# Kernel optimization log

Measured on AMD Instinct MI355X. Metric: run time of the kernel, lower is better.

## Reference

```python
import jax, jax.numpy as jnp
import numpy as np

N_NODES = 50000
N_EDGES = 200000
N_GRAPHS = 256
D_IN = 100
H = 384
STEPS = 4
EPS = 1e-5  # torch BatchNorm1d default eps


def setup_inputs() -> dict:
    key = jax.random.key(0)
    ks = jax.random.split(key, 16)
    def nrm(k, shape, s=0.05):
        return jax.random.normal(k, shape, jnp.float32) * s
    return {
        "x": jax.random.normal(ks[0], (N_NODES, D_IN), jnp.float32),
        "edge_index": jax.random.randint(ks[1], (2, N_EDGES), 0, N_NODES, jnp.int32),
        "batch": jnp.sort(jax.random.randint(ks[2], (N_NODES,), 0, N_GRAPHS, jnp.int32)),
        "w_in": nrm(ks[3], (D_IN, H)), "b_in": jnp.zeros((H,), jnp.float32),
        "bn1_g": jnp.ones((H,), jnp.float32), "bn1_b": jnp.zeros((H,), jnp.float32),
        "ggc_w": nrm(ks[4], (STEPS, H, H)),
        "gru_wih": nrm(ks[5], (3 * H, H)), "gru_whh": nrm(ks[6], (3 * H, H)),
        "gru_bih": jnp.zeros((3 * H,), jnp.float32), "gru_bhh": jnp.zeros((3 * H,), jnp.float32),
        "bn2_g": jnp.ones((H,), jnp.float32), "bn2_b": jnp.zeros((H,), jnp.float32),
        "att_w": nrm(ks[7], (H, 1)), "att_b": jnp.zeros((1,), jnp.float32),
        "fc1_w": nrm(ks[8], (H, H)), "fc1_b": jnp.zeros((H,), jnp.float32),
        "bn3_g": jnp.ones((H,), jnp.float32), "bn3_b": jnp.zeros((H,), jnp.float32),
        "fc2_w": nrm(ks[9], (H, H // 2)), "fc2_b": jnp.zeros((H // 2,), jnp.float32),
        "bn4_g": jnp.ones((H // 2,), jnp.float32), "bn4_b": jnp.zeros((H // 2,), jnp.float32),
        "fc3_w": nrm(ks[10], (H // 2, 2)), "fc3_b": jnp.zeros((2,), jnp.float32),
    }


def _bn(x, g, b):
    # training-mode BatchNorm1d: biased batch stats over dim 0
    m = x.mean(0)
    v = x.var(0)
    return (x - m) * jax.lax.rsqrt(v + EPS) * g + b


def reference(x, edge_index, batch, w_in, b_in, bn1_g, bn1_b, ggc_w,
              gru_wih, gru_whh, gru_bih, gru_bhh, bn2_g, bn2_b,
              att_w, att_b, fc1_w, fc1_b, bn3_g, bn3_b,
              fc2_w, fc2_b, bn4_g, bn4_b, fc3_w, fc3_b):
    h = jax.nn.relu(_bn(x @ w_in + b_in, bn1_g, bn1_b))  # [N, H]
    skip = h
    src, dst = edge_index[0], edge_index[1]
    # GatedGraphConv: per-step linear -> scatter-add over edges -> GRUCell
    for i in range(STEPS):
        m = h @ ggc_w[i]                                   # [N, H]
        agg = jax.ops.segment_sum(m[src], dst, num_segments=N_NODES)
        gi = agg @ gru_wih.T + gru_bih                     # [N, 3H]
        gh = h @ gru_whh.T + gru_bhh
        ir, iz, inn = jnp.split(gi, 3, axis=1)
        hr, hz, hn = jnp.split(gh, 3, axis=1)
        r = jax.nn.sigmoid(ir + hr)
        z = jax.nn.sigmoid(iz + hz)
        n = jnp.tanh(inn + r * hn)
        h = (1.0 - z) * n + z * h
    h = jax.nn.relu(_bn(h, bn2_g, bn2_b) + skip)
    # per-graph attention pooling (segment softmax + weighted segment sum)
    logits = (h @ att_w + att_b)[:, 0]                     # [N]
    seg_max = jax.ops.segment_max(logits, batch, num_segments=N_GRAPHS)
    e = jnp.exp(logits - seg_max[batch])
    denom = jax.ops.segment_sum(e, batch, num_segments=N_GRAPHS)
    w = e / denom[batch]
    pooled = jax.ops.segment_sum(w[:, None] * h, batch, num_segments=N_GRAPHS)  # [G, H]
    y = jax.nn.relu(_bn(pooled @ fc1_w + fc1_b, bn3_g, bn3_b))
    y = jax.nn.relu(_bn(y @ fc2_w + fc2_b, bn4_g, bn4_b))
    return y @ fc3_w + fc3_b                               # [G, 2]
```

## Files before the change

kernel.cpp:

```cpp
#include <hip/hip_runtime.h>
#include <math.h>

#define N_NODESC 50000
#define N_EDGESC 200000
#define N_GRAPHSC 256
#define D_INC 100
#define HD 384
#define STEPSC 4
#define BN_EPS 1e-5f

#define FPSCALE 4194304.0f
#define FPINV   (1.0f / 4194304.0f)

#define STATS_ROWS 512
#define STATS_BLOCKS 98

typedef _Float16 h8v __attribute__((ext_vector_type(8)));
typedef _Float16 h4v __attribute__((ext_vector_type(4)));
typedef float f4v __attribute__((ext_vector_type(4)));

static __device__ __forceinline__ float sigmoidf_(float x) { return 1.0f / (1.0f + expf(-x)); }

static __device__ __forceinline__ f4v mfma3(h8v ah, h8v al, h8v bh, h8v bl, f4v c) {
    c = __builtin_amdgcn_mfma_f32_16x16x32_f16(ah, bh, c, 0, 0, 0);
    c = __builtin_amdgcn_mfma_f32_16x16x32_f16(ah, bl, c, 0, 0, 0);
    c = __builtin_amdgcn_mfma_f32_16x16x32_f16(al, bh, c, 0, 0, 0);
    return c;
}

static __device__ __forceinline__ void gload_lds16(const _Float16* g, _Float16* l) {
    __builtin_amdgcn_global_load_lds(
        (const __attribute__((address_space(1))) unsigned int*)g,
        (__attribute__((address_space(3))) unsigned int*)l, 16, 0, 0);
}

static __device__ __forceinline__ int xcd_swz(int orig, int nwg) {
    const int q = nwg >> 3, r = nwg & 7;
    const int xcd = orig & 7, idx = orig >> 3;
    return (xcd < r ? xcd * (q + 1) : r * (q + 1) + (xcd - r) * q) + idx;
}

__global__ __launch_bounds__(256) void gemm64(const float* __restrict__ A,
                                              const float* __restrict__ B,
                                              const float* __restrict__ bias,
                                              float* __restrict__ C,
                                              int M, int K, int N) {
    __shared__ float As[16][68];
    __shared__ float Bs[16][68];
    const int tid = threadIdx.x;
    const int tx = tid & 15, ty = tid >> 4;
    const int m0 = blockIdx.y << 6, n0 = blockIdx.x << 6;
    const int ar = tid >> 2, ac4 = tid & 3;
    const int br = tid >> 4, bc4 = tid & 15;
    float acc[4][4] = {};
    for (int k0 = 0; k0 < K; k0 += 16) {
        float4 av = make_float4(0.f, 0.f, 0.f, 0.f);
        const int arow = m0 + ar, ak = k0 + (ac4 << 2);
        if (arow < M && ak < K) av = *(const float4*)(A + (size_t)arow * K + ak);
        As[(ac4 << 2) + 0][ar] = av.x;
        As[(ac4 << 2) + 1][ar] = av.y;
        As[(ac4 << 2) + 2][ar] = av.z;
        As[(ac4 << 2) + 3][ar] = av.w;
        float4 bv = make_float4(0.f, 0.f, 0.f, 0.f);
        const int bk = k0 + br;
        if (bk < K) bv = *(const float4*)(B + (size_t)bk * N + n0 + (bc4 << 2));
        *(float4*)&Bs[br][bc4 << 2] = bv;
        __syncthreads();
#pragma unroll
        for (int kk = 0; kk < 16; ++kk) {
            const float4 a = *(const float4*)&As[kk][ty << 2];
            const float4 b = *(const float4*)&Bs[kk][tx << 2];
            const float aarr[4] = {a.x, a.y, a.z, a.w};
            const float barr[4] = {b.x, b.y, b.z, b.w};
#pragma unroll
            for (int i = 0; i < 4; ++i)
#pragma unroll
                for (int j = 0; j < 4; ++j) acc[i][j] = fmaf(aarr[i], barr[j], acc[i][j]);
        }
        __syncthreads();
    }
#pragma unroll
    for (int i = 0; i < 4; ++i) {
        const int row = m0 + (ty << 2) + i;
        if (row >= M) continue;
        const int col0 = n0 + (tx << 2);
        float4 out;
        out.x = acc[i][0]; out.y = acc[i][1]; out.z = acc[i][2]; out.w = acc[i][3];
        if (bias) {
            out.x += bias[col0 + 0]; out.y += bias[col0 + 1];
            out.z += bias[col0 + 2]; out.w += bias[col0 + 3];
        }
        *(float4*)(C + (size_t)row * N + col0) = out;
    }
}


__global__ __launch_bounds__(256) void pack_gru_w(const float* __restrict__ w,
                                                  _Float16* __restrict__ PH,
                                                  _Float16* __restrict__ PL) {
    const int i = blockIdx.x * 256 + threadIdx.x;
    if (i >= 3 * 24 * 12 * 64) return;
    const int l = i & 63;
    const int kc = (i >> 6) % 12;
    const int jt = ((i >> 6) / 12) % 24;
    const int g = (i >> 6) / (12 * 24);
    const int row = g * HD + jt * 16 + (l & 15);
    const int k0 = kc * 32 + ((l >> 4) << 3);
    const float* s = w + (size_t)row * HD + k0;
    h8v hi, lo;
#pragma unroll
    for (int e = 0; e < 8; ++e) {
        const float v = s[e];
        hi[e] = (_Float16)v;
        lo[e] = (_Float16)(v - (float)hi[e]);
    }
    *(h8v*)(PH + (size_t)i * 8) = hi;
    *(h8v*)(PL + (size_t)i * 8) = lo;
}

__global__ __launch_bounds__(256) void pack_ggc_w(const float* __restrict__ w,
                                                  _Float16* __restrict__ PH,
                                                  _Float16* __restrict__ PL) {
    const int i = blockIdx.x * 256 + threadIdx.x;
    if (i >= STEPSC * 24 * 12 * 64) return;
    const int l = i & 63;
    const int kc = (i >> 6) % 12;
    const int jt = ((i >> 6) / 12) % 24;
    const int s = (i >> 6) / (12 * 24);
    const int n = jt * 16 + (l & 15);
    const int k0 = kc * 32 + ((l >> 4) << 3);
    h8v hi, lo;
#pragma unroll
    for (int e = 0; e < 8; ++e) {
        const float v = w[((size_t)s * HD + k0 + e) * HD + n];
        hi[e] = (_Float16)v;
        lo[e] = (_Float16)(v - (float)hi[e]);
    }
    *(h8v*)(PH + (size_t)i * 8) = hi;
    *(h8v*)(PL + (size_t)i * 8) = lo;
}

__global__ void deg_count(const int* __restrict__ dst, int* __restrict__ deg) {
    const int e = blockIdx.x * 256 + threadIdx.x;
    if (e < N_EDGESC) atomicAdd(&deg[dst[e]], 1);
}

__global__ __launch_bounds__(1024) void scan_deg(const int* __restrict__ deg,
                                                 int* __restrict__ offs) {
    __shared__ int sums[1024];
    const int t = threadIdx.x;
    const int CH = (N_NODESC + 1023) / 1024;
    const int base = t * CH;
    int s = 0;
    for (int i = 0; i < CH; ++i) {
        const int idx = base + i;
        if (idx < N_NODESC) s += deg[idx];
    }
    sums[t] = s;
    __syncthreads();
    for (int o = 1; o < 1024; o <<= 1) {
        const int v = (t >= o) ? sums[t - o] : 0;
        __syncthreads();
        sums[t] += v;
        __syncthreads();
    }
    int run = (t > 0) ? sums[t - 1] : 0;
    for (int i = 0; i < CH; ++i) {
        const int idx = base + i;
        if (idx < N_NODESC) {
            offs[idx] = run;
            run += deg[idx];
        }
    }
    if (t == 1023) offs[N_NODESC] = run;
}

__global__ void fill_csr(const int* __restrict__ src, const int* __restrict__ dst,
                         const int* __restrict__ offs, int* __restrict__ cursor,
                         int* __restrict__ esrc) {
    const int e = blockIdx.x * 256 + threadIdx.x;
    if (e >= N_EDGESC) return;
    const int d = dst[e];
    const int pos = atomicAdd(&cursor[d], 1);
    esrc[offs[d] + pos] = src[e];
}

__global__ __launch_bounds__(256) void gather_agg(const float* __restrict__ m,
                                                  const int* __restrict__ offs,
                                                  const int* __restrict__ esrc,
                                                  int* __restrict__ aggi) {
    const int gid = blockIdx.x * 256 + threadIdx.x;
    const int n = gid / 96;
    const int c = gid % 96;
    if (n >= N_NODESC) return;
    const int beg = offs[n], end = offs[n + 1];
    int4 acc = make_int4(0, 0, 0, 0);
    for (int i = beg; i < end; ++i) {
        const int s = esrc[i];
        const float4 v = *(const float4*)(m + (size_t)s * HD + (c << 2));
        acc.x += __float2int_rn(v.x * FPSCALE);
        acc.y += __float2int_rn(v.y * FPSCALE);
        acc.z += __float2int_rn(v.z * FPSCALE);
        acc.w += __float2int_rn(v.w * FPSCALE);
    }
    *(int4*)(aggi + (size_t)n * HD + (c << 2)) = acc;
}

__global__ __launch_bounds__(256) void ggc_lds(const _Float16* __restrict__ hH,
                                               const _Float16* __restrict__ hL,
                                               const _Float16* __restrict__ wtH,
                                               const _Float16* __restrict__ wtL,
                                               float* __restrict__ m) {
    __shared__ _Float16 sH[2][2][64][64];
    const int tid = threadIdx.x;
    const int wid = tid >> 6, lane = tid & 63;
    const int lr = lane & 15, lk = lane >> 4;
    const int wr = wid >> 1, wc = wid & 1;
    const int wgid = xcd_swz(blockIdx.x, gridDim.x);
    const int row0 = (wgid / 6) << 6, j0 = (wgid % 6) << 6;
    const int sp = wid >> 1;
    const int srbase = (wid & 1) << 5;
    const int lrow = lane >> 3, ls = lane & 7;
    const _Float16* splane = sp ? hL : hH;

    f4v acc[2][2];
    const f4v z4 = {0.f, 0.f, 0.f, 0.f};
    acc[0][0] = z4; acc[0][1] = z4; acc[1][0] = z4; acc[1][1] = z4;

#define GGC_STAGE(BUF, K0)                                                     \
    _Pragma("unroll")                                                          \
    for (int t4 = 0; t4 < 4; ++t4) {                                           \
        const int row = srbase + (t4 << 3) + lrow;                             \
        const int gk = (K0) + ((ls ^ (row & 7)) << 3);                         \
        const int grow = min(row0 + row, N_NODESC - 1);                        \
        gload_lds16(splane + (size_t)grow * HD + gk,                           \
                    &sH[BUF][sp][srbase + (t4 << 3)][0]);                      \
    }

    GGC_STAGE(0, 0);
    __syncthreads();
    int cur = 0;
    for (int t = 0; t < HD / 64; ++t) {
        if (t + 1 < HD / 64) GGC_STAGE(cur ^ 1, (t + 1) * 64);
#pragma unroll
        for (int kk = 0; kk < 64; kk += 32) {
            h8v fh[2], fl[2], bh[2], bl[2];
#pragma unroll
            for (int sm = 0; sm < 2; ++sm) {
                const int row = wr * 32 + sm * 16 + lr;
                const int s8 = (((kk >> 3) + lk) ^ (row & 7)) << 3;
                fh[sm] = *(const h8v*)&sH[cur][0][row][s8];
                fl[sm] = *(const h8v*)&sH[cur][1][row][s8];
            }
            const int kc = t * 2 + (kk >> 5);
#pragma unroll
            for (int sn = 0; sn < 2; ++sn) {
                const int jt = (j0 >> 4) + wc * 2 + sn;
                const size_t woff = ((size_t)(jt * 12 + kc) << 9) + (lane << 3);
                bh[sn] = *(const h8v*)(wtH + woff);
                bl[sn] = *(const h8v*)(wtL + woff);
            }
#pragma unroll
            for (int sm = 0; sm < 2; ++sm)
#pragma unroll
                for (int sn = 0; sn < 2; ++sn)
                    acc[sm][sn] = mfma3(fh[sm], fl[sm], bh[sn], bl[sn], acc[sm][sn]);
        }
        __syncthreads();
        cur ^= 1;
    }
#pragma unroll
    for (int sm = 0; sm < 2; ++sm)
#pragma unroll
        for (int sn = 0; sn < 2; ++sn) {
            const int col = j0 + wc * 32 + sn * 16 + lr;
#pragma unroll
            for (int j = 0; j < 4; ++j) {
                const int row = row0 + wr * 32 + sm * 16 + lk * 4 + j;
                if (row < N_NODESC) m[(size_t)row * HD + col] = acc[sm][sn][j];
            }
        }
#undef GGC_STAGE
}

__global__ __launch_bounds__(256) void gru_lds(const _Float16* __restrict__ aH,
                                               const _Float16* __restrict__ aL,
                                               const _Float16* __restrict__ hH,
                                               const _Float16* __restrict__ hL,
                                               const _Float16* __restrict__ wihH,
                                               const _Float16* __restrict__ wihL,
                                               const _Float16* __restrict__ whhH,
                                               const _Float16* __restrict__ whhL,
                                               const float* __restrict__ bih,
                                               const float* __restrict__ bhh,
                                               _Float16* __restrict__ oH,
                                               _Float16* __restrict__ oL) {
    __shared__ _Float16 sA[2][4][64][64];
    const int tid = threadIdx.x;
    const int wid = tid >> 6, lane = tid & 63;
    const int lr = lane & 15, lk = lane >> 4;
    const int wr = wid >> 1, wc = wid & 1;
    const int wgid = xcd_swz(blockIdx.x, gridDim.x);
    const int row0 = (wgid / 6) << 6, j0 = (wgid % 6) << 6;
    const int lrow = lane >> 3, ls = lane & 7;
    const _Float16* splane = (wid == 0) ? aH : (wid == 1) ? aL : (wid == 2) ? hH : hL;

    f4v acc[4][2][2];
    const f4v z4 = {0.f, 0.f, 0.f, 0.f};
#pragma unroll
    for (int g = 0; g < 4; ++g)
#pragma unroll
        for (int a = 0; a < 2; ++a)
#pragma unroll
            for (int b = 0; b < 2; ++b) acc[g][a][b] = z4;

#define GRU_STAGE(BUF, K0)                                                     \
    _Pragma("unroll")                                                          \
    for (int t8 = 0; t8 < 8; ++t8) {                                           \
        const int row = (t8 << 3) + lrow;                                      \
        const int gk = (K0) + ((ls ^ (row & 7)) << 3);                         \
        const int grow = min(row0 + row, N_NODESC - 1);                        \
        gload_lds16(splane + (size_t)grow * HD + gk,                           \
                    &sA[BUF][wid][t8 << 3][0]);                                \
    }

    GRU_STAGE(0, 0);
    __syncthreads();
    int cur = 0;
    for (int t = 0; t < HD / 64; ++t) {
        if (t + 1 < HD / 64) GRU_STAGE(cur ^ 1, (t + 1) * 64);
#pragma unroll
        for (int kk = 0; kk < 64; kk += 32) {
            h8v fAh[2], fAl[2], fHh[2], fHl[2];
#pragma unroll
            for (int sm = 0; sm < 2; ++sm) {
                const int row = wr * 32 + sm * 16 + lr;
                const int s8 = (((kk >> 3) + lk) ^ (row & 7)) << 3;
                fAh[sm] = *(const h8v*)&sA[cur][0][row][s8];
                fAl[sm] = *(const h8v*)&sA[cur][1][row][s8];
                fHh[sm] = *(const h8v*)&sA[cur][2][row][s8];
                fHl[sm] = *(const h8v*)&sA[cur][3][row][s8];
            }
            const int kc = t * 2 + (kk >> 5);
#pragma unroll
            for (int g = 0; g < 3; ++g) {
                h8v BiH[2], BiL[2], BhH[2], BhL[2];
#pragma unroll
                for (int sn = 0; sn < 2; ++sn) {
                    const int jt = (j0 >> 4) + wc * 2 + sn;
                    const size_t woff = ((size_t)((g * 24 + jt) * 12 + kc) << 9) + (lane << 3);
                    BiH[sn] = *(const h8v*)(wihH + woff);
                    BiL[sn] = *(const h8v*)(wihL + woff);
                    BhH[sn] = *(const h8v*)(whhH + woff);
                    BhL[sn] = *(const h8v*)(whhL + woff);
                }
                if (g < 2) {
#pragma unroll
                    for (int sm = 0; sm < 2; ++sm)
#pragma unroll
                        for (int sn = 0; sn < 2; ++sn) {
                            acc[g][sm][sn] = mfma3(fAh[sm], fAl[sm], BiH[sn], BiL[sn], acc[g][sm][sn]);
                            acc[g][sm][sn] = mfma3(fHh[sm], fHl[sm], BhH[sn], BhL[sn], acc[g][sm][sn]);
                        }
                } else {
#pragma unroll
                    for (int sm = 0; sm < 2; ++sm)
#pragma unroll
                        for (int sn = 0; sn < 2; ++sn) {
                            acc[2][sm][sn] = mfma3(fAh[sm], fAl[sm], BiH[sn], BiL[sn], acc[2][sm][sn]);
                            acc[3][sm][sn] = mfma3(fHh[sm], fHl[sm], BhH[sn], BhL[sn], acc[3][sm][sn]);
                        }
                }
            }
        }
        __syncthreads();
        cur ^= 1;
    }
#pragma unroll
    for (int sm = 0; sm < 2; ++sm)
#pragma unroll
        for (int sn = 0; sn < 2; ++sn) {
            const int col = j0 + wc * 32 + sn * 16 + lr;
            const float brz = bih[col] + bhh[col];
            const float bzz = bih[HD + col] + bhh[HD + col];
            const float bni = bih[2 * HD + col];
            const float bnh = bhh[2 * HD + col];
#pragma unroll
            for (int j = 0; j < 4; ++j) {
                const int row = row0 + wr * 32 + sm * 16 + lk * 4 + j;
                if (row < N_NODESC) {
                    const size_t off = (size_t)row * HD + col;
                    const float hold = (float)hH[off] + (float)hL[off];
                    const float r = sigmoidf_(acc[0][sm][sn][j] + brz);
                    const float z = sigmoidf_(acc[1][sm][sn][j] + bzz);
                    const float n = tanhf((acc[2][sm][sn][j] + bni) + r * (acc[3][sm][sn][j] + bnh));
                    const float res = (1.f - z) * n + z * hold;
                    const _Float16 hh = (_Float16)res;
                    oH[off] = hh;
                    oL[off] = (_Float16)(res - (float)hh);
                }
            }
        }
#undef GRU_STAGE
}

__global__ __launch_bounds__(256) void split_agg(const int* __restrict__ aggi,
                                                 _Float16* __restrict__ hi,
                                                 _Float16* __restrict__ lo) {
    const size_t i = (size_t)blockIdx.x * 256 + threadIdx.x;
    const int4 q = ((const int4*)aggi)[i];
    h4v a, b;
    float v;
    v = q.x * FPINV; a[0] = (_Float16)v; b[0] = (_Float16)(v - (float)a[0]);
    v = q.y * FPINV; a[1] = (_Float16)v; b[1] = (_Float16)(v - (float)a[1]);
    v = q.z * FPINV; a[2] = (_Float16)v; b[2] = (_Float16)(v - (float)a[2]);
    v = q.w * FPINV; a[3] = (_Float16)v; b[3] = (_Float16)(v - (float)a[3]);
    *(h4v*)(hi + i * 4) = a;
    *(h4v*)(lo + i * 4) = b;
}

__global__ __launch_bounds__(384) void col_stats_partial(const float* __restrict__ X, int M,
                                                         float* __restrict__ pS,
                                                         float* __restrict__ pQ) {
    const int f = threadIdx.x;
    const int b = blockIdx.x;
    const int r0 = b * STATS_ROWS;
    const int r1 = min(r0 + STATS_ROWS, M);
    float s = 0.f, q = 0.f;
    for (int r = r0; r < r1; ++r) {
        const float v = X[(size_t)r * HD + f];
        s += v;
        q += v * v;
    }
    pS[b * HD + f] = s;
    pQ[b * HD + f] = q;
}

__global__ __launch_bounds__(384) void col_stats_h(const _Float16* __restrict__ hH,
                                                   const _Float16* __restrict__ hL, int M,
                                                   float* __restrict__ pS,
                                                   float* __restrict__ pQ) {
    const int f = threadIdx.x;
    const int b = blockIdx.x;
    const int r0 = b * STATS_ROWS;
    const int r1 = min(r0 + STATS_ROWS, M);
    float s = 0.f, q = 0.f;
    for (int r = r0; r < r1; ++r) {
        const size_t off = (size_t)r * HD + f;
        const float v = (float)hH[off] + (float)hL[off];
        s += v;
        q += v * v;
    }
    pS[b * HD + f] = s;
    pQ[b * HD + f] = q;
}

__global__ void bn_stats_final(const float* __restrict__ pS, const float* __restrict__ pQ,
                               const float* __restrict__ g, const float* __restrict__ b,
                               float* __restrict__ scale, float* __restrict__ shift, float invM) {
    const int f = threadIdx.x;
    float s = 0.f, q = 0.f;
    for (int blk = 0; blk < STATS_BLOCKS; ++blk) {
        s += pS[blk * HD + f];
        q += pQ[blk * HD + f];
    }
    const float mean = s * invM;
    const float var = q * invM - mean * mean;
    const float sc = g[f] * rsqrtf(var + BN_EPS);
    scale[f] = sc;
    shift[f] = b[f] - mean * sc;
}

__global__ __launch_bounds__(256) void bn_relu_split(const float* __restrict__ X,
                                                     const float* __restrict__ scale,
                                                     const float* __restrict__ shift,
                                                     _Float16* __restrict__ hH,
                                                     _Float16* __restrict__ hL) {
    const size_t i4 = (size_t)blockIdx.x * 256 + threadIdx.x;
    const int f = (int)((i4 * 4) % HD);
    const float4 v = ((const float4*)X)[i4];
    float r0 = fmaxf(fmaf(v.x, scale[f + 0], shift[f + 0]), 0.f);
    float r1 = fmaxf(fmaf(v.y, scale[f + 1], shift[f + 1]), 0.f);
    float r2 = fmaxf(fmaf(v.z, scale[f + 2], shift[f + 2]), 0.f);
    float r3 = fmaxf(fmaf(v.w, scale[f + 3], shift[f + 3]), 0.f);
    h4v a, b;
    a[0] = (_Float16)r0; b[0] = (_Float16)(r0 - (float)a[0]);
    a[1] = (_Float16)r1; b[1] = (_Float16)(r1 - (float)a[1]);
    a[2] = (_Float16)r2; b[2] = (_Float16)(r2 - (float)a[2]);
    a[3] = (_Float16)r3; b[3] = (_Float16)(r3 - (float)a[3]);
    *(h4v*)(hH + i4 * 4) = a;
    *(h4v*)(hL + i4 * 4) = b;
}

__global__ __launch_bounds__(256) void bn_relu_apply(const float* X,
                                                     const float* __restrict__ scale,
                                                     const float* __restrict__ shift,
                                                     float* h) {
    const size_t i4 = (size_t)blockIdx.x * 256 + threadIdx.x;
    const int f = (int)((i4 * 4) % HD);
    const float4 v = ((const float4*)X)[i4];
    float4 r;
    r.x = fmaxf(fmaf(v.x, scale[f + 0], shift[f + 0]), 0.f);
    r.y = fmaxf(fmaf(v.y, scale[f + 1], shift[f + 1]), 0.f);
    r.z = fmaxf(fmaf(v.z, scale[f + 2], shift[f + 2]), 0.f);
    r.w = fmaxf(fmaf(v.w, scale[f + 3], shift[f + 3]), 0.f);
    ((float4*)h)[i4] = r;
}

__global__ __launch_bounds__(256) void bn_skip_relu_h(const _Float16* __restrict__ hH,
                                                      const _Float16* __restrict__ hL,
                                                      const float* __restrict__ scale,
                                                      const float* __restrict__ shift,
                                                      const float* __restrict__ skip,
                                                      float* __restrict__ out) {
    const size_t i4 = (size_t)blockIdx.x * 256 + threadIdx.x;
    const int f = (int)((i4 * 4) % HD);
    const h4v a = *(const h4v*)(hH + i4 * 4);
    const h4v b = *(const h4v*)(hL + i4 * 4);
    const float4 s = ((const float4*)skip)[i4];
    float4 r;
    r.x = fmaxf(fmaf((float)a[0] + (float)b[0], scale[f + 0], shift[f + 0]) + s.x, 0.f);
    r.y = fmaxf(fmaf((float)a[1] + (float)b[1], scale[f + 1], shift[f + 1]) + s.y, 0.f);
    r.z = fmaxf(fmaf((float)a[2] + (float)b[2], scale[f + 2], shift[f + 2]) + s.z, 0.f);
    r.w = fmaxf(fmaf((float)a[3] + (float)b[3], scale[f + 3], shift[f + 3]) + s.w, 0.f);
    ((float4*)out)[i4] = r;
}

__global__ __launch_bounds__(64) void att_logits(const float* __restrict__ h2,
                                                 const float* __restrict__ att_w,
                                                 const float* __restrict__ att_b,
                                                 float* __restrict__ logits) {
    const int n = blockIdx.x;
    const int l = threadIdx.x;
    float acc = 0.f;
#pragma unroll
    for (int k = 0; k < HD; k += 64) acc += h2[(size_t)n * HD + k + l] * att_w[k + l];
#pragma unroll
    for (int o = 32; o > 0; o >>= 1) acc += __shfl_down(acc, o);
    if (l == 0) logits[n] = acc + att_b[0];
}

__global__ void count_graphs(const int* __restrict__ batch, int* __restrict__ counts) {
    const int n = blockIdx.x * 256 + threadIdx.x;
    if (n < N_NODESC) atomicAdd(&counts[batch[n]], 1);
}

__global__ void scan_offsets(const int* __restrict__ counts, int* __restrict__ offs) {
    __shared__ int tmp[N_GRAPHSC];
    const int t = threadIdx.x;
    tmp[t] = counts[t];
    __syncthreads();
    for (int o = 1; o < N_GRAPHSC; o <<= 1) {
        int v = (t >= o) ? tmp[t - o] : 0;
        __syncthreads();
        tmp[t] += v;
        __syncthreads();
    }
    offs[t] = tmp[t] - counts[t];
}

__global__ __launch_bounds__(384) void pool_graphs(const float* __restrict__ h2,
                                                   const float* __restrict__ logits,
                                                   const int* __restrict__ offs,
                                                   const int* __restrict__ counts,
                                                   float* __restrict__ pooled) {
    const int g = blockIdx.x;
    const int t = threadIdx.x;
    const int s = offs[g], c = counts[g], e = s + c;
    __shared__ float red[384];
    float mx = -1e30f;
    for (int n = s + t; n < e; n += 384) mx = fmaxf(mx, logits[n]);
    red[t] = mx;
    __syncthreads();
    if (t < 128) red[t] = fmaxf(red[t], fmaxf(red[t + 128], red[t + 256]));
    __syncthreads();
    for (int w = 64; w > 0; w >>= 1) {
        if (t < w) red[t] = fmaxf(red[t], red[t + w]);
        __syncthreads();
    }
    mx = red[0];
    __syncthreads();
    float sm = 0.f;
    for (int n = s + t; n < e; n += 384) sm += expf(logits[n] - mx);
    red[t] = sm;
    __syncthreads();
    if (t < 128) red[t] += red[t + 128] + red[t + 256];
    __syncthreads();
    for (int w = 64; w > 0; w >>= 1) {
        if (t < w) red[t] += red[t + w];
        __syncthreads();
    }
    const float denom = red[0];
    const float inv = (c > 0) ? 1.0f / denom : 0.0f;
    float acc = 0.f;
    for (int n = s; n < e; ++n) acc += expf(logits[n] - mx) * h2[(size_t)n * HD + t];
    pooled[(size_t)g * HD + t] = acc * inv;
}

__global__ void fc_small(const float* __restrict__ X, const float* __restrict__ W,
                         const float* __restrict__ bias, float* __restrict__ Y,
                         int K, int N) {
    const int m = blockIdx.x;
    const int n = threadIdx.x;
    if (n >= N) return;
    float acc = bias[n];
    for (int k = 0; k < K; ++k) acc += X[m * K + k] * W[k * N + n];
    Y[m * N + n] = acc;
}

__global__ void bn_small_relu(float* X, int M, int N,
                              const float* __restrict__ g, const float* __restrict__ b) {
    const int f = threadIdx.x;
    if (f >= N) return;
    float s = 0.f, q = 0.f;
    for (int r = 0; r < M; ++r) {
        const float v = X[r * N + f];
        s += v;
        q += v * v;
    }
    const float mean = s / M;
    const float var = q / M - mean * mean;
    const float sc = g[f] * rsqrtf(var + BN_EPS);
    const float sh = b[f] - mean * sc;
    for (int r = 0; r < M; ++r) X[r * N + f] = fmaxf(X[r * N + f] * sc + sh, 0.f);
}

extern "C" void kernel_launch(void* const* d_in, const int* in_sizes, int n_in,
                              void* d_out, int out_size, void* d_ws, size_t ws_size,
                              hipStream_t stream) {
    const float* x       = (const float*)d_in[0];
    const int*   eidx    = (const int*)d_in[1];
    const int*   batch   = (const int*)d_in[2];
    const float* w_in    = (const float*)d_in[3];
    const float* b_in    = (const float*)d_in[4];
    const float* bn1_g   = (const float*)d_in[5];
    const float* bn1_b   = (const float*)d_in[6];
    const float* ggc_w   = (const float*)d_in[7];
    const float* gru_wih = (const float*)d_in[8];
    const float* gru_whh = (const float*)d_in[9];
    const float* gru_bih = (const float*)d_in[10];
    const float* gru_bhh = (const float*)d_in[11];
    const float* bn2_g   = (const float*)d_in[12];
    const float* bn2_b   = (const float*)d_in[13];
    const float* att_w   = (const float*)d_in[14];
    const float* att_b   = (const float*)d_in[15];
    const float* fc1_w   = (const float*)d_in[16];
    const float* fc1_b   = (const float*)d_in[17];
    const float* bn3_g   = (const float*)d_in[18];
    const float* bn3_b   = (const float*)d_in[19];
    const float* fc2_w   = (const float*)d_in[20];
    const float* fc2_b   = (const float*)d_in[21];
    const float* bn4_g   = (const float*)d_in[22];
    const float* bn4_b   = (const float*)d_in[23];
    const float* fc3_w   = (const float*)d_in[24];
    const float* fc3_b   = (const float*)d_in[25];

    const int* src = eidx;
    const int* dst = eidx + N_EDGESC;

    const size_t NH = (size_t)N_NODESC * HD;
    char* p = (char*)d_ws;
    float* R0 = (float*)p; p += NH * sizeof(float);
    float* R1 = (float*)p; p += NH * sizeof(float);
    float* Mreg = (float*)p; p += NH * sizeof(float);
    _Float16* wihP_H = (_Float16*)p; p += 3 * HD * HD * sizeof(_Float16);
    _Float16* wihP_L = (_Float16*)p; p += 3 * HD * HD * sizeof(_Float16);
    _Float16* whhP_H = (_Float16*)p; p += 3 * HD * HD * sizeof(_Float16);
    _Float16* whhP_L = (_Float16*)p; p += 3 * HD * HD * sizeof(_Float16);
    _Float16* ggcP_H = (_Float16*)p; p += (size_t)STEPSC * HD * HD * sizeof(_Float16);
    _Float16* ggcP_L = (_Float16*)p; p += (size_t)STEPSC * HD * HD * sizeof(_Float16);
    float* logits = (float*)p; p += N_NODESC * sizeof(float);
    float* pS = (float*)p; p += STATS_BLOCKS * HD * sizeof(float);
    float* pQ = (float*)p; p += STATS_BLOCKS * HD * sizeof(float);
    float* scale  = (float*)p; p += HD * sizeof(float);
    float* shift  = (float*)p; p += HD * sizeof(float);
    float* scale1 = (float*)p; p += HD * sizeof(float);
    float* shift1 = (float*)p; p += HD * sizeof(float);
    float* pooled = (float*)p; p += N_GRAPHSC * HD * sizeof(float);
    float* y1 = (float*)p; p += N_GRAPHSC * HD * sizeof(float);
    float* y2 = (float*)p; p += N_GRAPHSC * (HD / 2) * sizeof(float);
    int* counts = (int*)p; p += N_GRAPHSC * sizeof(int);
    int* offs = (int*)p; p += N_GRAPHSC * sizeof(int);
    int* deg    = (int*)p; p += N_NODESC * sizeof(int);
    int* eoffs  = (int*)p; p += (N_NODESC + 1) * sizeof(int);
    int* cursor = (int*)p; p += N_NODESC * sizeof(int);
    int* esrc   = (int*)p; p += N_EDGESC * sizeof(int);

    const int nwg = (HD / 64) * ((N_NODESC + 63) / 64);
    const int ew_blocks = (int)(NH / 4 / 256);

    hipMemsetAsync(deg, 0, N_NODESC * sizeof(int), stream);
    hipMemsetAsync(cursor, 0, N_NODESC * sizeof(int), stream);
    deg_count<<<(N_EDGESC + 255) / 256, 256, 0, stream>>>(dst, deg);
    scan_deg<<<1, 1024, 0, stream>>>(deg, eoffs);
    fill_csr<<<(N_EDGESC + 255) / 256, 256, 0, stream>>>(src, dst, eoffs, cursor, esrc);

    pack_gru_w<<<(3 * 24 * 12 * 64 + 255) / 256, 256, 0, stream>>>(gru_wih, wihP_H, wihP_L);
    pack_gru_w<<<(3 * 24 * 12 * 64 + 255) / 256, 256, 0, stream>>>(gru_whh, whhP_H, whhP_L);
    pack_ggc_w<<<(STEPSC * 24 * 12 * 64 + 255) / 256, 256, 0, stream>>>(ggc_w, ggcP_H, ggcP_L);

    gemm64<<<dim3(HD / 64, (N_NODESC + 63) / 64), 256, 0, stream>>>(x, w_in, b_in, R0,
                                                                    N_NODESC, D_INC, HD);
    col_stats_partial<<<STATS_BLOCKS, 384, 0, stream>>>(R0, N_NODESC, pS, pQ);
    bn_stats_final<<<1, 384, 0, stream>>>(pS, pQ, bn1_g, bn1_b, scale1, shift1, 1.0f / N_NODESC);
    bn_relu_split<<<ew_blocks, 256, 0, stream>>>(R0, scale1, shift1, (_Float16*)R1,
                                                 (_Float16*)R1 + NH);

    float* Hcur = R1;
    float* Oth = R0;
    _Float16* aggH = (_Float16*)Mreg;
    _Float16* aggL = aggH + NH;
    for (int s7 = 0; s7 < STEPSC; ++s7) {
        const _Float16* hcH = (const _Float16*)Hcur;
        const _Float16* hcL = (const _Float16*)Hcur + NH;
        ggc_lds<<<nwg, 256, 0, stream>>>(hcH, hcL,
                                         ggcP_H + (size_t)s7 * HD * HD,
                                         ggcP_L + (size_t)s7 * HD * HD, Mreg);
        gather_agg<<<(N_NODESC * 96 + 255) / 256, 256, 0, stream>>>(Mreg, eoffs, esrc, (int*)Oth);
        split_agg<<<ew_blocks, 256, 0, stream>>>((const int*)Oth, aggH, aggL);
        gru_lds<<<nwg, 256, 0, stream>>>(aggH, aggL, hcH, hcL, wihP_H, wihP_L, whhP_H, whhP_L,
                                         gru_bih, gru_bhh,
                                         (_Float16*)Oth, (_Float16*)Oth + NH);
        float* t = Hcur; Hcur = Oth; Oth = t;
    }

    const _Float16* hfH = (const _Float16*)Hcur;
    const _Float16* hfL = (const _Float16*)Hcur + NH;
    col_stats_h<<<STATS_BLOCKS, 384, 0, stream>>>(hfH, hfL, N_NODESC, pS, pQ);
    bn_stats_final<<<1, 384, 0, stream>>>(pS, pQ, bn2_g, bn2_b, scale, shift, 1.0f / N_NODESC);
    gemm64<<<dim3(HD / 64, (N_NODESC + 63) / 64), 256, 0, stream>>>(x, w_in, b_in, Oth,
                                                                    N_NODESC, D_INC, HD);
    bn_relu_apply<<<ew_blocks, 256, 0, stream>>>(Oth, scale1, shift1, Oth);
    float* hfinal = Mreg;
    bn_skip_relu_h<<<ew_blocks, 256, 0, stream>>>(hfH, hfL, scale, shift, Oth, hfinal);

    att_logits<<<N_NODESC, 64, 0, stream>>>(hfinal, att_w, att_b, logits);
    hipMemsetAsync(counts, 0, N_GRAPHSC * sizeof(int), stream);
    count_graphs<<<(N_NODESC + 255) / 256, 256, 0, stream>>>(batch, counts);
    scan_offsets<<<1, N_GRAPHSC, 0, stream>>>(counts, offs);
    pool_graphs<<<N_GRAPHSC, 384, 0, stream>>>(hfinal, logits, offs, counts, pooled);

    fc_small<<<N_GRAPHSC, 384, 0, stream>>>(pooled, fc1_w, fc1_b, y1, HD, HD);
    bn_small_relu<<<1, 384, 0, stream>>>(y1, N_GRAPHSC, HD, bn3_g, bn3_b);
    fc_small<<<N_GRAPHSC, 192, 0, stream>>>(y1, fc2_w, fc2_b, y2, HD, HD / 2);
    bn_small_relu<<<1, 192, 0, stream>>>(y2, N_GRAPHSC, HD / 2, bn4_g, bn4_b);
    fc_small<<<N_GRAPHSC, 64, 0, stream>>>(y2, fc3_w, fc3_b, (float*)d_out, HD / 2, 2);
}
```

Baseline: 3.190 ms.

## Store messages as fp16 hi/lo pairs, fuse split into gather, raise MFMA priority

The GGC GEMM now writes its message matrix as fp16 hi/lo planes instead of fp32. The edge gather reads these 8-wide fp16 vectors, accumulates in fixed point, and converts directly to the hi/lo agg planes, which removes the separate split_agg kernel and its int32 round trip. Buffers are reassigned so the messages live in Oth and the GRU output overwrites them. s_setprio is also raised around the MFMA blocks in both GEMM kernels. The ggc epilogue now does scalar fp16 stores, and buffer aliasing across steps must hold for correctness.

```diff
diff --git a/kernel.cpp b/kernel.cpp
--- a/kernel.cpp
+++ b/kernel.cpp
@@ -185,32 +185,44 @@
     esrc[offs[d] + pos] = src[e];
 }
 
-__global__ __launch_bounds__(256) void gather_agg(const float* __restrict__ m,
-                                                  const int* __restrict__ offs,
-                                                  const int* __restrict__ esrc,
-                                                  int* __restrict__ aggi) {
+__global__ __launch_bounds__(256) void gather_agg_h(const _Float16* __restrict__ mH,
+                                                    const _Float16* __restrict__ mL,
+                                                    const int* __restrict__ offs,
+                                                    const int* __restrict__ esrc,
+                                                    _Float16* __restrict__ aggH,
+                                                    _Float16* __restrict__ aggL) {
     const int gid = blockIdx.x * 256 + threadIdx.x;
-    const int n = gid / 96;
-    const int c = gid % 96;
+    const int n = gid / 48;
+    const int c = gid % 48;
     if (n >= N_NODESC) return;
     const int beg = offs[n], end = offs[n + 1];
-    int4 acc = make_int4(0, 0, 0, 0);
+    int acc[8] = {};
     for (int i = beg; i < end; ++i) {
         const int s = esrc[i];
-        const float4 v = *(const float4*)(m + (size_t)s * HD + (c << 2));
-        acc.x += __float2int_rn(v.x * FPSCALE);
-        acc.y += __float2int_rn(v.y * FPSCALE);
-        acc.z += __float2int_rn(v.z * FPSCALE);
-        acc.w += __float2int_rn(v.w * FPSCALE);
-    }
-    *(int4*)(aggi + (size_t)n * HD + (c << 2)) = acc;
+        const size_t so = (size_t)s * HD + (c << 3);
+        const h8v vh = *(const h8v*)(mH + so);
+        const h8v vl = *(const h8v*)(mL + so);
+#pragma unroll
+        for (int j = 0; j < 8; ++j)
+            acc[j] += __float2int_rn(((float)vh[j] + (float)vl[j]) * FPSCALE);
+    }
+    h8v a, b;
+#pragma unroll
+    for (int j = 0; j < 8; ++j) {
+        const float v = acc[j] * FPINV;
+        a[j] = (_Float16)v;
+        b[j] = (_Float16)(v - (float)a[j]);
+    }
+    *(h8v*)(aggH + (size_t)n * HD + (c << 3)) = a;
+    *(h8v*)(aggL + (size_t)n * HD + (c << 3)) = b;
 }
 
 __global__ __launch_bounds__(256) void ggc_lds(const _Float16* __restrict__ hH,
                                                const _Float16* __restrict__ hL,
                                                const _Float16* __restrict__ wtH,
                                                const _Float16* __restrict__ wtL,
-                                               float* __restrict__ m) {
+                                               _Float16* __restrict__ mH,
+                                               _Float16* __restrict__ mL) {
     __shared__ _Float16 sH[2][2][64][64];
     const int tid = threadIdx.x;
     const int wid = tid >> 6, lane = tid & 63;
@@ -260,11 +272,13 @@
                 bh[sn] = *(const h8v*)(wtH + woff);
                 bl[sn] = *(const h8v*)(wtL + woff);
             }
+            __builtin_amdgcn_s_setprio(1);
 #pragma unroll
             for (int sm = 0; sm < 2; ++sm)
 #pragma unroll
                 for (int sn = 0; sn < 2; ++sn)
                     acc[sm][sn] = mfma3(fh[sm], fl[sm], bh[sn], bl[sn], acc[sm][sn]);
+            __builtin_amdgcn_s_setprio(0);
         }
         __syncthreads();
         cur ^= 1;
@@ -277,7 +291,13 @@
 #pragma unroll
             for (int j = 0; j < 4; ++j) {
                 const int row = row0 + wr * 32 + sm * 16 + lk * 4 + j;
-                if (row < N_NODESC) m[(size_t)row * HD + col] = acc[sm][sn][j];
+                if (row < N_NODESC) {
+                    const size_t off = (size_t)row * HD + col;
+                    const float v = acc[sm][sn][j];
+                    const _Float16 hh = (_Float16)v;
+                    mH[off] = hh;
+                    mL[off] = (_Float16)(v - (float)hh);
+                }
             }
         }
 #undef GGC_STAGE
@@ -354,6 +374,7 @@
                     BhH[sn] = *(const h8v*)(whhH + woff);
                     BhL[sn] = *(const h8v*)(whhL + woff);
                 }
+                __builtin_amdgcn_s_setprio(1);
                 if (g < 2) {
 #pragma unroll
                     for (int sm = 0; sm < 2; ++sm)
@@ -371,6 +392,7 @@
                             acc[3][sm][sn] = mfma3(fHh[sm], fHl[sm], BhH[sn], BhL[sn], acc[3][sm][sn]);
                         }
                 }
+                __builtin_amdgcn_s_setprio(0);
             }
         }
         __syncthreads();
@@ -402,21 +424,6 @@
             }
         }
 #undef GRU_STAGE
-}
-
-__global__ __launch_bounds__(256) void split_agg(const int* __restrict__ aggi,
-                                                 _Float16* __restrict__ hi,
-                                                 _Float16* __restrict__ lo) {
-    const size_t i = (size_t)blockIdx.x * 256 + threadIdx.x;
-    const int4 q = ((const int4*)aggi)[i];
-    h4v a, b;
-    float v;
-    v = q.x * FPINV; a[0] = (_Float16)v; b[0] = (_Float16)(v - (float)a[0]);
-    v = q.y * FPINV; a[1] = (_Float16)v; b[1] = (_Float16)(v - (float)a[1]);
-    v = q.z * FPINV; a[2] = (_Float16)v; b[2] = (_Float16)(v - (float)a[2]);
-    v = q.w * FPINV; a[3] = (_Float16)v; b[3] = (_Float16)(v - (float)a[3]);
-    *(h4v*)(hi + i * 4) = a;
-    *(h4v*)(lo + i * 4) = b;
 }
 
 __global__ __launch_bounds__(384) void col_stats_partial(const float* __restrict__ X, int M,
@@ -713,14 +720,15 @@
     for (int s7 = 0; s7 < STEPSC; ++s7) {
         const _Float16* hcH = (const _Float16*)Hcur;
         const _Float16* hcL = (const _Float16*)Hcur + NH;
+        _Float16* mH = (_Float16*)Oth;
+        _Float16* mL = mH + NH;
         ggc_lds<<<nwg, 256, 0, stream>>>(hcH, hcL,
                                          ggcP_H + (size_t)s7 * HD * HD,
-                                         ggcP_L + (size_t)s7 * HD * HD, Mreg);
-        gather_agg<<<(N_NODESC * 96 + 255) / 256, 256, 0, stream>>>(Mreg, eoffs, esrc, (int*)Oth);
-        split_agg<<<ew_blocks, 256, 0, stream>>>((const int*)Oth, aggH, aggL);
+                                         ggcP_L + (size_t)s7 * HD * HD, mH, mL);
+        gather_agg_h<<<(N_NODESC * 48) / 256 + 1, 256, 0, stream>>>(mH, mL, eoffs, esrc,
+                                                                    aggH, aggL);
         gru_lds<<<nwg, 256, 0, stream>>>(aggH, aggL, hcH, hcL, wihP_H, wihP_L, whhP_H, whhP_L,
-                                         gru_bih, gru_bhh,
-                                         (_Float16*)Oth, (_Float16*)Oth + NH);
+                                         gru_bih, gru_bhh, mH, mL);
         float* t = Hcur; Hcur = Oth; Oth = t;
     }
 
```

After: 2.989 ms. -6.3%, faster.
